# Kernel optimization log

Hardware: AMD Instinct MI355X
Metric: run time of the kernel (lower is better)

The kernel has to match this reference:

```python
import jax, jax.numpy as jnp
import numpy as np

N_NODES = 100000
N_EDGES = 1600000
D = 64


def _gcn_norm(edge_index, edge_weight, num_nodes):
    # PyG GCNConv default: add self-loops (weight 1), symmetric deg^-1/2 norm.
    src, dst = edge_index[0], edge_index[1]
    loop = jnp.arange(num_nodes, dtype=edge_index.dtype)
    src = jnp.concatenate([src, loop])
    dst = jnp.concatenate([dst, loop])
    w = jnp.concatenate([edge_weight, jnp.ones((num_nodes,), edge_weight.dtype)])
    deg = jax.ops.segment_sum(w, dst, num_segments=num_nodes)
    dinv = jnp.where(deg > 0, jax.lax.rsqrt(deg), 0.0)
    norm = dinv[src] * w * dinv[dst]  # [E + N]
    return src, dst, norm


def _gcn_conv(h, src, dst, norm, W, b, num_nodes):
    h = h @ W                                   # [N, C_out] linear transform first
    msg = h[src] * norm[:, None]                # gather + scale  [E+N, C_out]
    out = jax.ops.segment_sum(msg, dst, num_segments=num_nodes)  # scatter-add
    return out + b


def setup_inputs() -> dict:
    key = jax.random.key(0)
    ks = jax.random.split(key, 9)
    x = jax.random.normal(ks[0], (N_NODES, D), dtype=jnp.float32)
    edge_index = jax.random.randint(ks[1], (2, N_EDGES), 0, N_NODES, dtype=jnp.int32)
    edge_weight = jax.random.uniform(ks[2], (N_EDGES,), dtype=jnp.float32)
    s = 1.0 / np.sqrt(D)
    W1 = jax.random.uniform(ks[3], (D, D), jnp.float32, -s, s)
    b1 = jnp.zeros((D,), jnp.float32)
    W2 = jax.random.uniform(ks[4], (D, D), jnp.float32, -s, s)
    b2 = jnp.zeros((D,), jnp.float32)
    W3 = jax.random.uniform(ks[5], (D, 1), jnp.float32, -s, s)
    b3 = jnp.zeros((1,), jnp.float32)
    return {"x": x, "edge_index": edge_index, "edge_weight": edge_weight,
            "W1": W1, "b1": b1, "W2": W2, "b2": b2, "W3": W3, "b3": b3}


def reference(x, edge_index, edge_weight, W1, b1, W2, b2, W3, b3):
    n = x.shape[0]
    src, dst, norm = _gcn_norm(edge_index, edge_weight, n)
    h = _gcn_conv(x, src, dst, norm, W1, b1, n)
    h = jax.nn.relu(h)
    h = _gcn_conv(h, src, dst, norm, W2, b2, n)
    h = jax.nn.relu(h)
    h = _gcn_conv(h, src, dst, norm, W3, b3, n)
    return jax.nn.sigmoid(h)  # [N, 1]
```

## Files before the change

### kernel.cpp

```cpp
#include <hip/hip_runtime.h>
#include <hip/hip_fp16.h>
#include <math.h>

#define NN 100000
#define NE 1600000
#define D 64
#define BSH 8
#define NBIN 391
#define EB 8192
#define NBB ((NE + EB - 1) / EB)

typedef _Float16 f16x8 __attribute__((ext_vector_type(8)));
typedef float f32x4 __attribute__((ext_vector_type(4)));

__global__ void k_binhist(const int* __restrict__ dst, int* __restrict__ counts, int E) {
    __shared__ int h[NBIN];
    for (int i = threadIdx.x; i < NBIN; i += blockDim.x) h[i] = 0;
    __syncthreads();
    int e0 = blockIdx.x * EB;
    int e1 = min(e0 + EB, E);
    for (int e = e0 + threadIdx.x; e < e1; e += blockDim.x)
        atomicAdd(&h[dst[e] >> BSH], 1);
    __syncthreads();
    for (int i = threadIdx.x; i < NBIN; i += blockDim.x)
        counts[blockIdx.x * NBIN + i] = h[i];
}

__global__ void k_binscan(int* __restrict__ counts, int* __restrict__ binStart) {
    __shared__ int tot[512];
    int b = threadIdx.x;
    int sum = 0;
    if (b < NBIN) {
#pragma unroll 8
        for (int k = 0; k < NBB; k++) {
            int idx = k * NBIN + b;
            int c = counts[idx];
            counts[idx] = sum;
            sum += c;
        }
    }
    tot[b] = (b < NBIN) ? sum : 0;
    __syncthreads();
    int v = tot[b];
    for (int off = 1; off < 512; off <<= 1) {
        int add = (b >= off) ? tot[b - off] : 0;
        __syncthreads();
        tot[b] += add;
        __syncthreads();
    }
    if (b < NBIN) binStart[b] = tot[b] - v;
    if (b == NBIN - 1) binStart[NBIN] = tot[b];
}

__global__ void k_binscatter(const int* __restrict__ src, const int* __restrict__ dst,
                             const float* __restrict__ w, const int* __restrict__ counts,
                             const int* __restrict__ binStart, int2* __restrict__ binned,
                             int E) {
    __shared__ int cur[NBIN];
    for (int i = threadIdx.x; i < NBIN; i += blockDim.x)
        cur[i] = binStart[i] + counts[blockIdx.x * NBIN + i];
    __syncthreads();
    int e0 = blockIdx.x * EB;
    int e1 = min(e0 + EB, E);
    for (int e = e0 + threadIdx.x; e < e1; e += blockDim.x) {
        int d = dst[e];
        int pos = atomicAdd(&cur[d >> BSH], 1);
        binned[pos] = make_int2(((d & 255) << 17) | src[e], __float_as_int(w[e]));
    }
}

__global__ void k_deg(const int2* __restrict__ binned, const int* __restrict__ binStart,
                      float* __restrict__ dinv, int* __restrict__ row_ptr, int n) {
    __shared__ int   cnt[256];
    __shared__ float ws[256];
    __shared__ int   off[256];
    int b = blockIdx.x, t = threadIdx.x;
    cnt[t] = 0; ws[t] = 0.0f;
    __syncthreads();
    int e0 = binStart[b], e1 = binStart[b + 1];
    for (int e = e0 + t; e < e1; e += 256) {
        int2 r = binned[e];
        int dlow = (unsigned)r.x >> 17;
        atomicAdd(&cnt[dlow], 1);
        atomicAdd(&ws[dlow], __int_as_float(r.y));
    }
    __syncthreads();
    int v = cnt[t];
    off[t] = v;
    __syncthreads();
    for (int o = 1; o < 256; o <<= 1) {
        int add = (t >= o) ? off[t - o] : 0;
        __syncthreads();
        off[t] += add;
        __syncthreads();
    }
    int node = b * 256 + t;
    if (node < n) {
        dinv[node] = rsqrtf(1.0f + ws[t]);
        row_ptr[node] = e0 + off[t] - v;
    }
    if (b == NBIN - 1 && t == 0) row_ptr[n] = binStart[NBIN];
}

__global__ void k_csr(const int2* __restrict__ binned, const int* __restrict__ binStart,
                      const int* __restrict__ row_ptr, const float* __restrict__ dinv,
                      int2* __restrict__ edges, int n) {
    __shared__ int   rp[256];
    __shared__ int   cur[256];
    __shared__ float dd[256];
    int b = blockIdx.x, t = threadIdx.x;
    int node = b * 256 + t;
    rp[t]  = (node < n) ? row_ptr[node] : 0;
    dd[t]  = (node < n) ? dinv[node] : 0.0f;
    cur[t] = 0;
    __syncthreads();
    int e0 = binStart[b], e1 = binStart[b + 1];
    for (int e = e0 + t; e < e1; e += 256) {
        int2 r = binned[e];
        int dlow = (unsigned)r.x >> 17;
        int s = r.x & 0x1FFFF;
        int rank = atomicAdd(&cur[dlow], 1);
        float nv = dinv[s] * __int_as_float(r.y) * dd[dlow];
        edges[rp[dlow] + rank] = make_int2(s, __float_as_int(nv));
    }
}

template <int IN_HALF>
__global__ void k_gemm(const void* __restrict__ Xv, const float* __restrict__ W,
                       __half* __restrict__ T, int n) {
    int wid = (int)((blockIdx.x * blockDim.x + threadIdx.x) >> 6);
    int lane = threadIdx.x & 63;
    int col16 = lane & 15, kg = lane >> 4;
    int r0 = wid * 32;
    if (r0 >= n) return;
    f16x8 bf[2][4];
#pragma unroll
    for (int kk = 0; kk < 2; kk++)
#pragma unroll
        for (int ct = 0; ct < 4; ct++) {
            f16x8 b;
#pragma unroll
            for (int j = 0; j < 8; j++)
                b[j] = (_Float16)W[(size_t)(kk * 32 + kg * 8 + j) * D + ct * 16 + col16];
            bf[kk][ct] = b;
        }
#pragma unroll
    for (int tt = 0; tt < 2; tt++) {
        int row = r0 + tt * 16 + col16;
        f16x8 a0, a1;
        if (IN_HALF) {
            const _Float16* xr = (const _Float16*)Xv + (size_t)row * D;
            a0 = *(const f16x8*)(xr + kg * 8);
            a1 = *(const f16x8*)(xr + 32 + kg * 8);
        } else {
            const float* xr = (const float*)Xv + (size_t)row * D;
#pragma unroll
            for (int j = 0; j < 8; j++) {
                a0[j] = (_Float16)xr[kg * 8 + j];
                a1[j] = (_Float16)xr[32 + kg * 8 + j];
            }
        }
#pragma unroll
        for (int ct = 0; ct < 4; ct++) {
            f32x4 z = {0.0f, 0.0f, 0.0f, 0.0f};
            z = __builtin_amdgcn_mfma_f32_16x16x32_f16(a0, bf[0][ct], z, 0, 0, 0);
            z = __builtin_amdgcn_mfma_f32_16x16x32_f16(a1, bf[1][ct], z, 0, 0, 0);
            __half* to = T + (size_t)(r0 + tt * 16 + kg * 4) * D + ct * 16 + col16;
#pragma unroll
            for (int r = 0; r < 4; r++)
                to[(size_t)r * D] = __float2half(z[r]);
        }
    }
}

template <int FUSE_W3>
__global__ void k_agg(const __half2* __restrict__ T2, const int* __restrict__ row_ptr,
                      const int2* __restrict__ edges, const float* __restrict__ dinv,
                      const float* __restrict__ bias, const float* __restrict__ W3,
                      void* __restrict__ outv, int n) {
    int wave = (int)((blockIdx.x * blockDim.x + threadIdx.x) >> 6);
    int lane = threadIdx.x & 63;
    if (wave >= n) return;
    int c = lane & 31;
    int h = lane >> 5;
    int beg = row_ptr[wave], end = row_ptr[wave + 1];
    float ax = 0.0f, ay = 0.0f, bx = 0.0f, by = 0.0f;
    int i = beg;
    for (; i + 16 <= end; i += 16) {
        int2 er[8];
#pragma unroll
        for (int j = 0; j < 8; j++) er[j] = edges[i + 2 * j + h];
        __half2 tv[8];
#pragma unroll
        for (int j = 0; j < 8; j++) tv[j] = T2[(size_t)er[j].x * 32 + c];
#pragma unroll
        for (int j = 0; j < 8; j++) {
            float nv = __int_as_float(er[j].y);
            float2 f = __half22float2(tv[j]);
            if (j & 1) { bx += nv * f.x; by += nv * f.y; }
            else       { ax += nv * f.x; ay += nv * f.y; }
        }
    }
    if (i + 8 <= end) {
        int2 er[4];
#pragma unroll
        for (int j = 0; j < 4; j++) er[j] = edges[i + 2 * j + h];
        __half2 tv[4];
#pragma unroll
        for (int j = 0; j < 4; j++) tv[j] = T2[(size_t)er[j].x * 32 + c];
#pragma unroll
        for (int j = 0; j < 4; j++) {
            float nv = __int_as_float(er[j].y);
            float2 f = __half22float2(tv[j]);
            if (j & 1) { bx += nv * f.x; by += nv * f.y; }
            else       { ax += nv * f.x; ay += nv * f.y; }
        }
        i += 8;
    }
    if (i + 4 <= end) {
        int2 er[2];
#pragma unroll
        for (int j = 0; j < 2; j++) er[j] = edges[i + 2 * j + h];
#pragma unroll
        for (int j = 0; j < 2; j++) {
            float nv = __int_as_float(er[j].y);
            float2 f = __half22float2(T2[(size_t)er[j].x * 32 + c]);
            if (j & 1) { bx += nv * f.x; by += nv * f.y; }
            else       { ax += nv * f.x; ay += nv * f.y; }
        }
        i += 4;
    }
    if (i + 2 <= end) {
        int2 e = edges[i + h];
        float nv = __int_as_float(e.y);
        float2 f = __half22float2(T2[(size_t)e.x * 32 + c]);
        ax += nv * f.x; ay += nv * f.y;
        i += 2;
    }
    if (i < end && h == 0) {
        int2 e = edges[i];
        float nv = __int_as_float(e.y);
        float2 f = __half22float2(T2[(size_t)e.x * 32 + c]);
        ax += nv * f.x; ay += nv * f.y;
    }
    ax += bx; ay += by;
    ax += __shfl_xor(ax, 32);
    ay += __shfl_xor(ay, 32);
    float dv = dinv[wave];
    float2 self = __half22float2(T2[(size_t)wave * 32 + c]);
    float hx = fmaxf(ax + dv * dv * self.x + bias[2 * c], 0.0f);
    float hy = fmaxf(ay + dv * dv * self.y + bias[2 * c + 1], 0.0f);
    if (FUSE_W3) {
        float pp = hx * W3[2 * c] + hy * W3[2 * c + 1];
#pragma unroll
        for (int off = 16; off; off >>= 1) pp += __shfl_xor(pp, off);
        if (lane == 0) ((float*)outv)[wave] = pp;
    } else {
        if (lane < 32) ((__half2*)outv)[(size_t)wave * 32 + c] = __floats2half2_rn(hx, hy);
    }
}

__global__ void k_agg3(const float* __restrict__ t3, const int* __restrict__ row_ptr,
                       const int2* __restrict__ edges, const float* __restrict__ dinv,
                       const float* __restrict__ b3, float* __restrict__ out, int n) {
    int v = blockIdx.x * blockDim.x + threadIdx.x;
    if (v >= n) return;
    float dv = dinv[v];
    float acc0 = dv * dv * t3[v];
    float acc1 = 0.0f;
    int beg = row_ptr[v], end = row_ptr[v + 1];
    int i = beg;
    for (; i + 8 <= end; i += 8) {
        int2 er[8]; float av[8];
#pragma unroll
        for (int j = 0; j < 8; j++) er[j] = edges[i + j];
#pragma unroll
        for (int j = 0; j < 8; j++) av[j] = t3[er[j].x];
#pragma unroll
        for (int j = 0; j < 8; j++) {
            if (j & 1) acc1 += __int_as_float(er[j].y) * av[j];
            else       acc0 += __int_as_float(er[j].y) * av[j];
        }
    }
    for (; i < end; i++) {
        int2 e = edges[i];
        acc0 += __int_as_float(e.y) * t3[e.x];
    }
    float z = acc0 + acc1 + b3[0];
    out[v] = 1.0f / (1.0f + expf(-z));
}

extern "C" void kernel_launch(void* const* d_in, const int* in_sizes, int n_in,
                              void* d_out, int out_size, void* d_ws, size_t ws_size,
                              hipStream_t stream) {
    const float* x  = (const float*)d_in[0];
    const int*   ei = (const int*)d_in[1];
    const float* w  = (const float*)d_in[2];
    const float* W1 = (const float*)d_in[3];
    const float* b1 = (const float*)d_in[4];
    const float* W2 = (const float*)d_in[5];
    const float* b2 = (const float*)d_in[6];
    const float* W3 = (const float*)d_in[7];
    const float* b3 = (const float*)d_in[8];
    float* out = (float*)d_out;

    const int N = NN, E = NE;
    const int* src = ei;
    const int* dst = ei + E;

    char* p = (char*)d_ws;
    auto alloc = [&](size_t bytes) -> char* {
        char* r = p;
        p += (bytes + 255) & ~(size_t)255;
        return r;
    };
    float* dinv    = (float*)alloc((size_t)N * 4);
    int*   row_ptr = (int*)alloc((size_t)(N + 1) * 4);
    int*   binStart= (int*)alloc((NBIN + 1) * 4);
    int*   counts  = (int*)alloc((size_t)NBB * NBIN * 4);
    int2*  binned  = (int2*)alloc((size_t)E * 8);
    int2*  edges   = (int2*)alloc((size_t)E * 8);
    __half* bufA   = (__half*)alloc((size_t)N * D * 2);
    __half* bufB   = (__half*)alloc((size_t)N * D * 2);
    float* t3      = (float*)alloc((size_t)N * 4);

    const int BT = 256;
    int gN = (N + BT - 1) / BT;
    int gW = (N * 64 + BT - 1) / BT;
    int nWaves = (N + 31) / 32;
    int gG = (nWaves * 64 + BT - 1) / BT;

    k_binhist<<<NBB, BT, 0, stream>>>(dst, counts, E);
    k_binscan<<<1, 512, 0, stream>>>(counts, binStart);
    k_binscatter<<<NBB, BT, 0, stream>>>(src, dst, w, counts, binStart, binned, E);
    k_deg<<<NBIN, BT, 0, stream>>>(binned, binStart, dinv, row_ptr, N);
    k_csr<<<NBIN, BT, 0, stream>>>(binned, binStart, row_ptr, dinv, edges, N);

    k_gemm<0><<<gG, BT, 0, stream>>>(x, W1, bufA, N);
    k_agg<0><<<gW, BT, 0, stream>>>((const __half2*)bufA, row_ptr, edges, dinv, b1, nullptr, bufB, N);
    k_gemm<1><<<gG, BT, 0, stream>>>(bufB, W2, bufA, N);
    k_agg<1><<<gW, BT, 0, stream>>>((const __half2*)bufA, row_ptr, edges, dinv, b2, W3, t3, N);
    k_agg3<<<gN, BT, 0, stream>>>(t3, row_ptr, edges, dinv, b3, out, N);
}
```

Measured before the change: 226.3 us.

## Fold source-side degree normalization into GEMM output and fuse degree/CSR kernels

The symmetric norm is split so that edges store only w*dinv[dst]. The dinv[src] factor is applied once per node in the GEMM epilogue, and the self-loop and final-layer terms are adjusted to match. Because CSR construction no longer needs dinv of arbitrary source nodes, the degree and CSR kernels merge into one block-local kernel. That removes a launch and a random gather of dinv over all edges. Streaming edge and input reads also switch to nontemporal loads to reduce cache pollution, and the fp16 intermediates are now stored pre-scaled.

```diff
diff --git a/kernel.cpp b/kernel.cpp
--- a/kernel.cpp
+++ b/kernel.cpp
@@ -13,6 +13,14 @@
 typedef _Float16 f16x8 __attribute__((ext_vector_type(8)));
 typedef float f32x4 __attribute__((ext_vector_type(4)));
 
+__device__ __forceinline__ int2 ldnt2(const int2* p) {
+    unsigned long long r = __builtin_nontemporal_load((const unsigned long long*)p);
+    int2 o;
+    o.x = (int)(unsigned)(r & 0xffffffffu);
+    o.y = (int)(unsigned)(r >> 32);
+    return o;
+}
+
 __global__ void k_binhist(const int* __restrict__ dst, int* __restrict__ counts, int E) {
     __shared__ int h[NBIN];
     for (int i = threadIdx.x; i < NBIN; i += blockDim.x) h[i] = 0;
@@ -20,7 +28,7 @@
     int e0 = blockIdx.x * EB;
     int e1 = min(e0 + EB, E);
     for (int e = e0 + threadIdx.x; e < e1; e += blockDim.x)
-        atomicAdd(&h[dst[e] >> BSH], 1);
+        atomicAdd(&h[__builtin_nontemporal_load(dst + e) >> BSH], 1);
     __syncthreads();
     for (int i = threadIdx.x; i < NBIN; i += blockDim.x)
         counts[blockIdx.x * NBIN + i] = h[i];
@@ -63,17 +71,22 @@
     int e0 = blockIdx.x * EB;
     int e1 = min(e0 + EB, E);
     for (int e = e0 + threadIdx.x; e < e1; e += blockDim.x) {
-        int d = dst[e];
+        int d = __builtin_nontemporal_load(dst + e);
+        int s = __builtin_nontemporal_load(src + e);
+        float wv = __builtin_nontemporal_load(w + e);
         int pos = atomicAdd(&cur[d >> BSH], 1);
-        binned[pos] = make_int2(((d & 255) << 17) | src[e], __float_as_int(w[e]));
-    }
-}
-
-__global__ void k_deg(const int2* __restrict__ binned, const int* __restrict__ binStart,
-                      float* __restrict__ dinv, int* __restrict__ row_ptr, int n) {
+        binned[pos] = make_int2(((d & 255) << 17) | s, __float_as_int(wv));
+    }
+}
+
+__global__ void k_degcsr(const int2* __restrict__ binned, const int* __restrict__ binStart,
+                         float* __restrict__ dinv, int* __restrict__ row_ptr,
+                         int2* __restrict__ edges, int n) {
     __shared__ int   cnt[256];
     __shared__ float ws[256];
     __shared__ int   off[256];
+    __shared__ int   rp[256];
+    __shared__ float dd[256];
     int b = blockIdx.x, t = threadIdx.x;
     cnt[t] = 0; ws[t] = 0.0f;
     __syncthreads();
@@ -95,39 +108,26 @@
         __syncthreads();
     }
     int node = b * 256 + t;
-    if (node < n) {
-        dinv[node] = rsqrtf(1.0f + ws[t]);
-        row_ptr[node] = e0 + off[t] - v;
-    }
+    float dvv = rsqrtf(1.0f + ws[t]);
+    rp[t] = e0 + off[t] - v;
+    dd[t] = dvv;
+    if (node < n) { dinv[node] = dvv; row_ptr[node] = rp[t]; }
     if (b == NBIN - 1 && t == 0) row_ptr[n] = binStart[NBIN];
-}
-
-__global__ void k_csr(const int2* __restrict__ binned, const int* __restrict__ binStart,
-                      const int* __restrict__ row_ptr, const float* __restrict__ dinv,
-                      int2* __restrict__ edges, int n) {
-    __shared__ int   rp[256];
-    __shared__ int   cur[256];
-    __shared__ float dd[256];
-    int b = blockIdx.x, t = threadIdx.x;
-    int node = b * 256 + t;
-    rp[t]  = (node < n) ? row_ptr[node] : 0;
-    dd[t]  = (node < n) ? dinv[node] : 0.0f;
-    cur[t] = 0;
-    __syncthreads();
-    int e0 = binStart[b], e1 = binStart[b + 1];
+    cnt[t] = 0;
+    __syncthreads();
     for (int e = e0 + t; e < e1; e += 256) {
         int2 r = binned[e];
         int dlow = (unsigned)r.x >> 17;
         int s = r.x & 0x1FFFF;
-        int rank = atomicAdd(&cur[dlow], 1);
-        float nv = dinv[s] * __int_as_float(r.y) * dd[dlow];
+        int rank = atomicAdd(&cnt[dlow], 1);
+        float nv = __int_as_float(r.y) * dd[dlow];
         edges[rp[dlow] + rank] = make_int2(s, __float_as_int(nv));
     }
 }
 
 template <int IN_HALF>
 __global__ void k_gemm(const void* __restrict__ Xv, const float* __restrict__ W,
-                       __half* __restrict__ T, int n) {
+                       const float* __restrict__ dinv, __half* __restrict__ T, int n) {
     int wid = (int)((blockIdx.x * blockDim.x + threadIdx.x) >> 6);
     int lane = threadIdx.x & 63;
     int col16 = lane & 15, kg = lane >> 4;
@@ -160,6 +160,9 @@
                 a1[j] = (_Float16)xr[32 + kg * 8 + j];
             }
         }
+        float dvr[4];
+#pragma unroll
+        for (int r = 0; r < 4; r++) dvr[r] = dinv[r0 + tt * 16 + kg * 4 + r];
 #pragma unroll
         for (int ct = 0; ct < 4; ct++) {
             f32x4 z = {0.0f, 0.0f, 0.0f, 0.0f};
@@ -168,7 +171,7 @@
             __half* to = T + (size_t)(r0 + tt * 16 + kg * 4) * D + ct * 16 + col16;
 #pragma unroll
             for (int r = 0; r < 4; r++)
-                to[(size_t)r * D] = __float2half(z[r]);
+                to[(size_t)r * D] = __float2half(z[r] * dvr[r]);
         }
     }
 }
@@ -189,7 +192,7 @@
     for (; i + 16 <= end; i += 16) {
         int2 er[8];
 #pragma unroll
-        for (int j = 0; j < 8; j++) er[j] = edges[i + 2 * j + h];
+        for (int j = 0; j < 8; j++) er[j] = ldnt2(&edges[i + 2 * j + h]);
         __half2 tv[8];
 #pragma unroll
         for (int j = 0; j < 8; j++) tv[j] = T2[(size_t)er[j].x * 32 + c];
@@ -204,7 +207,7 @@
     if (i + 8 <= end) {
         int2 er[4];
 #pragma unroll
-        for (int j = 0; j < 4; j++) er[j] = edges[i + 2 * j + h];
+        for (int j = 0; j < 4; j++) er[j] = ldnt2(&edges[i + 2 * j + h]);
         __half2 tv[4];
 #pragma unroll
         for (int j = 0; j < 4; j++) tv[j] = T2[(size_t)er[j].x * 32 + c];
@@ -220,7 +223,7 @@
     if (i + 4 <= end) {
         int2 er[2];
 #pragma unroll
-        for (int j = 0; j < 2; j++) er[j] = edges[i + 2 * j + h];
+        for (int j = 0; j < 2; j++) er[j] = ldnt2(&edges[i + 2 * j + h]);
 #pragma unroll
         for (int j = 0; j < 2; j++) {
             float nv = __int_as_float(er[j].y);
@@ -231,14 +234,14 @@
         i += 4;
     }
     if (i + 2 <= end) {
-        int2 e = edges[i + h];
+        int2 e = ldnt2(&edges[i + h]);
         float nv = __int_as_float(e.y);
         float2 f = __half22float2(T2[(size_t)e.x * 32 + c]);
         ax += nv * f.x; ay += nv * f.y;
         i += 2;
     }
     if (i < end && h == 0) {
-        int2 e = edges[i];
+        int2 e = ldnt2(&edges[i]);
         float nv = __int_as_float(e.y);
         float2 f = __half22float2(T2[(size_t)e.x * 32 + c]);
         ax += nv * f.x; ay += nv * f.y;
@@ -248,13 +251,13 @@
     ay += __shfl_xor(ay, 32);
     float dv = dinv[wave];
     float2 self = __half22float2(T2[(size_t)wave * 32 + c]);
-    float hx = fmaxf(ax + dv * dv * self.x + bias[2 * c], 0.0f);
-    float hy = fmaxf(ay + dv * dv * self.y + bias[2 * c + 1], 0.0f);
+    float hx = fmaxf(ax + dv * self.x + bias[2 * c], 0.0f);
+    float hy = fmaxf(ay + dv * self.y + bias[2 * c + 1], 0.0f);
     if (FUSE_W3) {
         float pp = hx * W3[2 * c] + hy * W3[2 * c + 1];
 #pragma unroll
         for (int off = 16; off; off >>= 1) pp += __shfl_xor(pp, off);
-        if (lane == 0) ((float*)outv)[wave] = pp;
+        if (lane == 0) ((float*)outv)[wave] = dv * pp;
     } else {
         if (lane < 32) ((__half2*)outv)[(size_t)wave * 32 + c] = __floats2half2_rn(hx, hy);
     }
@@ -266,14 +269,14 @@
     int v = blockIdx.x * blockDim.x + threadIdx.x;
     if (v >= n) return;
     float dv = dinv[v];
-    float acc0 = dv * dv * t3[v];
+    float acc0 = dv * t3[v];
     float acc1 = 0.0f;
     int beg = row_ptr[v], end = row_ptr[v + 1];
     int i = beg;
     for (; i + 8 <= end; i += 8) {
         int2 er[8]; float av[8];
 #pragma unroll
-        for (int j = 0; j < 8; j++) er[j] = edges[i + j];
+        for (int j = 0; j < 8; j++) er[j] = ldnt2(&edges[i + j]);
 #pragma unroll
         for (int j = 0; j < 8; j++) av[j] = t3[er[j].x];
 #pragma unroll
@@ -283,7 +286,7 @@
         }
     }
     for (; i < end; i++) {
-        int2 e = edges[i];
+        int2 e = ldnt2(&edges[i]);
         acc0 += __int_as_float(e.y) * t3[e.x];
     }
     float z = acc0 + acc1 + b3[0];
@@ -333,12 +336,11 @@
     k_binhist<<<NBB, BT, 0, stream>>>(dst, counts, E);
     k_binscan<<<1, 512, 0, stream>>>(counts, binStart);
     k_binscatter<<<NBB, BT, 0, stream>>>(src, dst, w, counts, binStart, binned, E);
-    k_deg<<<NBIN, BT, 0, stream>>>(binned, binStart, dinv, row_ptr, N);
-    k_csr<<<NBIN, BT, 0, stream>>>(binned, binStart, row_ptr, dinv, edges, N);
-
-    k_gemm<0><<<gG, BT, 0, stream>>>(x, W1, bufA, N);
+    k_degcsr<<<NBIN, BT, 0, stream>>>(binned, binStart, dinv, row_ptr, edges, N);
+
+    k_gemm<0><<<gG, BT, 0, stream>>>(x, W1, dinv, bufA, N);
     k_agg<0><<<gW, BT, 0, stream>>>((const __half2*)bufA, row_ptr, edges, dinv, b1, nullptr, bufB, N);
-    k_gemm<1><<<gG, BT, 0, stream>>>(bufB, W2, bufA, N);
+    k_gemm<1><<<gG, BT, 0, stream>>>(bufB, W2, dinv, bufA, N);
     k_agg<1><<<gW, BT, 0, stream>>>((const __half2*)bufA, row_ptr, edges, dinv, b2, W3, t3, N);
     k_agg3<<<gN, BT, 0, stream>>>(t3, row_ptr, edges, dinv, b3, out, N);
 }
```

After: 223.7 us. About the same (-1.1%).
